# Kernel optimization log

Hardware: AMD Instinct MI355X
Metric: run time of the kernel (lower is better)

The kernel has to match this reference:

```python
import jax, jax.numpy as jnp
from jax import lax
import numpy as np

L, B, T, D, H = 4, 64, 256, 1024, 1024  # num_layers, batch, seq_len, input_dim, hidden_dim


def setup_inputs() -> dict:
    key = jax.random.key(0)
    ks = jax.random.split(key, 10)
    s = 0.05  # weight scale ~ xavier-ish for stability
    return {
        "x": jax.random.normal(ks[0], (B, T, D), jnp.float32),
        "hidden": jax.random.normal(ks[1], (L, B, H), jnp.float32),
        "cell": jax.random.normal(ks[2], (L, B, H), jnp.float32),
        # stacked per-layer LSTM params (layer0 input dim == H since D == H)
        "W_ih": jax.random.normal(ks[3], (L, 4 * H, H), jnp.float32) * s,
        "W_hh": jax.random.normal(ks[4], (L, 4 * H, H), jnp.float32) * s,
        "b": jax.random.normal(ks[5], (L, 4 * H), jnp.float32) * s,  # b_ih + b_hh combined
        "W_out": jax.random.normal(ks[6], (D, H), jnp.float32) * s,
        "b_out": jnp.zeros((D,), jnp.float32),
    }


def _lstm_layer(x_seq, h0, c0, Wih, Whh, b):
    """Run one LSTM layer over the full sequence.
    x_seq: [B,T,Din]; h0,c0: [B,H]. Returns hidden/cell sequences [B,T,H]."""
    # precompute input-side gate projections for all timesteps: [T,B,4H]
    gx = jnp.einsum('btd,gd->tbg', x_seq, Wih) + b

    def step(carry, gx_t):
        h, c = carry
        g = gx_t + h @ Whh.T  # [B,4H]
        i, f, gg, o = jnp.split(g, 4, axis=-1)  # torch gate order i,f,g,o
        c = jax.nn.sigmoid(f) * c + jax.nn.sigmoid(i) * jnp.tanh(gg)
        h = jax.nn.sigmoid(o) * jnp.tanh(c)
        return (h, c), (h, c)

    _, (hs, cs) = lax.scan(step, (h0, c0), gx)
    return jnp.swapaxes(hs, 0, 1), jnp.swapaxes(cs, 0, 1)  # [B,T,H]


def reference(x, hidden, cell, W_ih, W_hh, b, W_out, b_out):
    # dropout in eval mode (identity) for a deterministic reference
    out_h = x
    new_h, new_c = [], []
    for i in range(L):
        out_h, out_c = _lstm_layer(out_h, hidden[i], cell[i], W_ih[i], W_hh[i], b[i])
        new_h.append(out_h[:, -1])
        new_c.append(out_c[:, -1])
    logits = out_h @ W_out.T + b_out  # [B,T,D]
    return logits, (jnp.stack(new_h, axis=0), jnp.stack(new_c, axis=0))
```

## Files before the change

### kernel.cpp

```cpp
#include <hip/hip_runtime.h>
#include <cstdint>
#include <cstddef>


#define LL 4
#define BB 64
#define TT 256
#define DD 1024
#define HH 1024
#define FOURH 4096
#define APAD 1032
#define PPAD 68

typedef __bf16 bf16;
typedef __bf16 bf16x8 __attribute__((ext_vector_type(8)));
typedef __bf16 bf16x4 __attribute__((ext_vector_type(4)));
typedef __bf16 bf16x2 __attribute__((ext_vector_type(2)));
typedef float f32x4 __attribute__((ext_vector_type(4)));

__device__ __forceinline__ void async_load16(const void* g, void* l) {
    __builtin_amdgcn_global_load_lds(
        (const __attribute__((address_space(1))) unsigned int*)g,
        (__attribute__((address_space(3))) unsigned int*)l,
        16, 0, 0);
}

__device__ __forceinline__ f32x4 mfma_bf16(bf16x8 a, bf16x8 b, f32x4 c) {
    return __builtin_amdgcn_mfma_f32_16x16x32_bf16(a, b, c, 0, 0, 0);
}

__device__ __forceinline__ float fsig(float x) {
    return 1.f / (1.f + __expf(-x));
}
__device__ __forceinline__ float ftanh(float x) {
    x = fminf(10.f, fmaxf(-10.f, x));
    float e = __expf(2.f * x);
    return (e - 1.f) / (e + 1.f);
}

__device__ __forceinline__ int aload(const int* p) {
    return __hip_atomic_load(p, __ATOMIC_RELAXED, __HIP_MEMORY_SCOPE_AGENT);
}
__device__ __forceinline__ void astore(int* p, int v) {
    __hip_atomic_store(p, v, __ATOMIC_RELAXED, __HIP_MEMORY_SCOPE_AGENT);
}

__global__ void cvt_f32_bf16(const float* __restrict__ in, bf16* __restrict__ out, int n4) {
    int i = blockIdx.x * blockDim.x + threadIdx.x;
    if (i < n4) {
        float4 v = ((const float4*)in)[i];
        bf16x4 o = { (bf16)v.x, (bf16)v.y, (bf16)v.z, (bf16)v.w };
        ((bf16x4*)out)[i] = o;
    }
}

__global__ __launch_bounds__(256) void cvt_x_transpose(
    const float* __restrict__ x, bf16* __restrict__ out) {
    int bx = blockIdx.x;
    int b = bx >> 8, t = bx & 255;
    int tid = threadIdx.x;
    float4 v = ((const float4*)(x + (size_t)bx * DD))[tid];
    bf16x4 o = { (bf16)v.x, (bf16)v.y, (bf16)v.z, (bf16)v.w };
    ((bf16x4*)(out + ((size_t)(t * BB + b)) * DD))[tid] = o;
}

template <bool OUT_BF16, bool REMAP>
__global__ __launch_bounds__(256) void gemm_bt(
    const bf16* __restrict__ A, const bf16* __restrict__ W,
    const float* __restrict__ bias, void* __restrict__ Cout,
    int M, int N, int K)
{
    __shared__ bf16 As[128 * 32];
    __shared__ bf16 Bs[128 * 32];
    const int tid = threadIdx.x;
    const int wave = tid >> 6, lane = tid & 63;
    const int lmod = lane & 15, lhalf = lane >> 4;
    const int m0 = blockIdx.y * 128, n0 = blockIdx.x * 128;
    const int wr = (wave >> 1) * 64, wc = (wave & 1) * 64;

    f32x4 acc[4][4] = {};

    const int arow = tid >> 2;
    const int acol = (tid & 3) * 8;
    const bf16* Ab  = A + (size_t)(m0 + arow) * K + acol;
    const bf16* Ab2 = A + (size_t)(m0 + 64 + arow) * K + acol;
    const bf16* Wb  = W + (size_t)(n0 + arow) * K + acol;
    const bf16* Wb2 = W + (size_t)(n0 + 64 + arow) * K + acol;

    for (int kc = 0; kc < K; kc += 32) {
        async_load16(Ab + kc,  &As[tid * 8]);
        async_load16(Ab2 + kc, &As[2048 + tid * 8]);
        async_load16(Wb + kc,  &Bs[tid * 8]);
        async_load16(Wb2 + kc, &Bs[2048 + tid * 8]);
        __syncthreads();

        bf16x8 af[4], bfr[4];
#pragma unroll
        for (int mt = 0; mt < 4; mt++)
            af[mt] = *(const bf16x8*)&As[(wr + mt * 16 + lmod) * 32 + lhalf * 8];
#pragma unroll
        for (int nt = 0; nt < 4; nt++)
            bfr[nt] = *(const bf16x8*)&Bs[(wc + nt * 16 + lmod) * 32 + lhalf * 8];
#pragma unroll
        for (int mt = 0; mt < 4; mt++)
#pragma unroll
            for (int nt = 0; nt < 4; nt++)
                acc[mt][nt] = mfma_bf16(af[mt], bfr[nt], acc[mt][nt]);
        __syncthreads();
    }

#pragma unroll
    for (int mt = 0; mt < 4; mt++) {
#pragma unroll
        for (int nt = 0; nt < 4; nt++) {
            int n = n0 + wc + nt * 16 + lmod;
            float bv = bias[n];
#pragma unroll
            for (int r = 0; r < 4; r++) {
                int m = m0 + wr + mt * 16 + lhalf * 4 + r;
                int orow = REMAP ? ((m & 63) * TT + (m >> 6)) : m;
                float v = acc[mt][nt][r] + bv;
                if (OUT_BF16)
                    ((bf16*)Cout)[(size_t)orow * N + n] = (bf16)v;
                else
                    ((float*)Cout)[(size_t)orow * N + n] = v;
            }
        }
    }
}

__global__ __launch_bounds__(256, 1) void lstm_pipe(
    const bf16* __restrict__ x_bf,
    const bf16* __restrict__ h0_all,
    const float* __restrict__ c0_all,
    const bf16* __restrict__ wih,
    const bf16* __restrict__ whh,
    const float* __restrict__ bias,
    bf16* __restrict__ hseq_base,
    float* __restrict__ outH, float* __restrict__ outC,
    int* __restrict__ flags,
    int* __restrict__ mbox)
{
    __shared__ __align__(16) unsigned char smem_raw[64 * APAD * 2];
    bf16*  As = (bf16*)smem_raw;
    float* P  = (float*)smem_raw;

    const int tid = threadIdx.x;
    const int wave = tid >> 6, lane = tid & 63;
    const int lmod = lane & 15, lhalf = lane >> 4;
    const int bid = blockIdx.x;
    const int layer = bid >> 6;
    const int j0 = (bid & 63) * 16;
    const bool isAgg = ((bid & 63) == 0);

    const size_t SLAB = (size_t)TT * BB * HH;
    const bf16* inseq = (layer == 0) ? x_bf : (hseq_base + (size_t)(layer - 1) * SLAB);
    bf16* hseq = hseq_base + (size_t)layer * SLAB;
    const bf16* h0 = h0_all + (size_t)layer * BB * HH;
    const float* c0 = c0_all + (size_t)layer * BB * HH;
    float* oH = outH + (size_t)layer * BB * HH;
    float* oC = outC + (size_t)layer * BB * HH;

    bf16x8 wI[4][8], wH[4][8];
    {
        const size_t lbase = (size_t)layer * FOURH;
#pragma unroll
        for (int nt = 0; nt < 4; nt++) {
            const bf16* rI = wih + (lbase + nt * 1024 + j0 + lmod) * 1024
                                 + wave * 256 + lhalf * 8;
            const bf16* rH = whh + (lbase + nt * 1024 + j0 + lmod) * 1024
                                 + wave * 256 + lhalf * 8;
#pragma unroll
            for (int kc = 0; kc < 8; kc++) {
                wI[nt][kc] = *(const bf16x8*)(rI + kc * 32);
                wH[nt][kc] = *(const bf16x8*)(rH + kc * 32);
            }
        }
    }

    const int jj0 = (tid * 2) & 15;
    float bj[4][2];
#pragma unroll
    for (int g = 0; g < 4; g++) {
        bj[g][0] = bias[layer * FOURH + g * 1024 + j0 + jj0];
        bj[g][1] = bias[layer * FOURH + g * 1024 + j0 + jj0 + 1];
    }

    float2 creg[2];
#pragma unroll
    for (int q = 0; q < 2; q++) {
        int p = q * 512 + tid * 2;
        creg[q] = *(const float2*)&c0[(p >> 4) * 1024 + j0 + (p & 15)];
    }

    auto stage = [&](const bf16* src) {
#pragma unroll
        for (int i = 0; i < 32; i++) {
            int k = wave * 32 + i;
            int row = k >> 1, half = k & 1;
            async_load16(src + (size_t)row * 1024 + half * 512 + lane * 8,
                         &As[row * APAD + half * 512 + lane * 8]);
        }
    };

    for (int t = 0; t < TT; t++) {
        if (wave == 0) {
            if (isAgg && t > 0) {
                for (;;) {
                    int v = aload(&flags[layer * 64 + lane]);
                    if (__all(v >= t)) break;
                }
                astore(&mbox[(layer * 64 + lane) * 16 + 0], t);
                if (layer < 3)
                    astore(&mbox[((layer + 1) * 64 + lane) * 16 + 1], t);
            }
            if (layer > 0 && lane == 0) {
                while (aload(&mbox[bid * 16 + 1]) < t + 1) {}
            }
        }
        __syncthreads();

        stage(inseq + (size_t)t * (BB * HH));
        __syncthreads();

        f32x4 acc[4][4] = {};
#pragma unroll
        for (int kc = 0; kc < 8; kc++) {
            bf16x8 af[4];
#pragma unroll
            for (int mt = 0; mt < 4; mt++)
                af[mt] = *(const bf16x8*)&As[(mt * 16 + lmod) * APAD
                                             + wave * 256 + kc * 32 + lhalf * 8];
#pragma unroll
            for (int mt = 0; mt < 4; mt++)
#pragma unroll
                for (int nt = 0; nt < 4; nt++)
                    acc[mt][nt] = mfma_bf16(af[mt], wI[nt][kc], acc[mt][nt]);
        }

        if (wave == 0 && !isAgg && t > 0 && lane == 0) {
            while (aload(&mbox[bid * 16 + 0]) < t) {}
        }
        __syncthreads();

        stage((t == 0) ? h0 : (hseq + (size_t)(t - 1) * BB * HH));
        __syncthreads();

#pragma unroll
        for (int kc = 0; kc < 8; kc++) {
            bf16x8 af[4];
#pragma unroll
            for (int mt = 0; mt < 4; mt++)
                af[mt] = *(const bf16x8*)&As[(mt * 16 + lmod) * APAD
                                             + wave * 256 + kc * 32 + lhalf * 8];
#pragma unroll
            for (int mt = 0; mt < 4; mt++)
#pragma unroll
                for (int nt = 0; nt < 4; nt++)
                    acc[mt][nt] = mfma_bf16(af[mt], wH[nt][kc], acc[mt][nt]);
        }
        __syncthreads();

#pragma unroll
        for (int mt = 0; mt < 4; mt++)
#pragma unroll
            for (int nt = 0; nt < 4; nt++)
#pragma unroll
                for (int rr = 0; rr < 4; rr++) {
                    int m = mt * 16 + lhalf * 4 + rr;
                    P[(wave * 64 + m) * PPAD + nt * 16 + lmod] = acc[mt][nt][rr];
                }
        __syncthreads();

        const bool lastt = (t == TT - 1);
#pragma unroll
        for (int q = 0; q < 2; q++) {
            int p = q * 512 + tid * 2;
            int m = p >> 4, jj = p & 15;
            float gg4[4][2];
#pragma unroll
            for (int g = 0; g < 4; g++) {
                float s0 = bj[g][0], s1 = bj[g][1];
#pragma unroll
                for (int w = 0; w < 4; w++) {
                    float2 pv = *(const float2*)&P[(w * 64 + m) * PPAD + g * 16 + jj];
                    s0 += pv.x; s1 += pv.y;
                }
                gg4[g][0] = s0; gg4[g][1] = s1;
            }
            float cv[2], hv[2];
#pragma unroll
            for (int u = 0; u < 2; u++) {
                float gi = gg4[0][u], gf = gg4[1][u], gc = gg4[2][u], go = gg4[3][u];
                float cprev = u ? creg[q].y : creg[q].x;
                float c = fsig(gf) * cprev + fsig(gi) * ftanh(gc);
                float h = fsig(go) * ftanh(c);
                cv[u] = c; hv[u] = h;
            }
            creg[q].x = cv[0]; creg[q].y = cv[1];
            union { bf16x2 h2; unsigned int u32; } pk;
            pk.h2.x = (bf16)hv[0]; pk.h2.y = (bf16)hv[1];
            __hip_atomic_store(
                (unsigned int*)&hseq[((size_t)(t * BB + m)) * HH + j0 + jj],
                pk.u32, __ATOMIC_RELAXED, __HIP_MEMORY_SCOPE_AGENT);
            if (lastt) {
                *(float2*)&oH[m * 1024 + j0 + jj] = make_float2(hv[0], hv[1]);
                *(float2*)&oC[m * 1024 + j0 + jj] = make_float2(cv[0], cv[1]);
            }
        }

        __syncthreads();
        if (tid == 0) astore(&flags[bid], t + 1);
    }

    if (wave == 0 && isAgg && layer < 3) {
        for (;;) {
            int v = aload(&flags[layer * 64 + lane]);
            if (__all(v >= TT)) break;
        }
        astore(&mbox[((layer + 1) * 64 + lane) * 16 + 1], TT);
    }
}

extern "C" void kernel_launch(void* const* d_in, const int* in_sizes, int n_in,
                              void* d_out, int out_size, void* d_ws, size_t ws_size,
                              hipStream_t stream) {
    const float* x    = (const float*)d_in[0];
    const float* h0   = (const float*)d_in[1];
    const float* c0   = (const float*)d_in[2];
    const float* Wih  = (const float*)d_in[3];
    const float* Whh  = (const float*)d_in[4];
    const float* bias = (const float*)d_in[5];
    const float* Wout = (const float*)d_in[6];
    const float* bout = (const float*)d_in[7];

    char* p = (char*)d_ws;
    int*  ctrs    = (int*)p;  p += 1024;
    int*  mbox    = (int*)p;  p += 256 * 64;
    bf16* x_bf    = (bf16*)p; p += (size_t)BB * TT * DD * 2;
    bf16* hseq    = (bf16*)p; p += (size_t)LL * BB * TT * HH * 2;
    bf16* wih_bf  = (bf16*)p; p += (size_t)LL * FOURH * HH * 2;
    bf16* whh_bf  = (bf16*)p; p += (size_t)LL * FOURH * HH * 2;
    bf16* wout_bf = (bf16*)p; p += (size_t)DD * HH * 2;
    bf16* h0_bf   = (bf16*)p; p += (size_t)LL * BB * HH * 2;
    if ((size_t)(p - (char*)d_ws) > ws_size) return;

    hipMemsetAsync(ctrs, 0, 1024 + 256 * 64, stream);

    cvt_x_transpose<<<BB * TT, 256, 0, stream>>>(x, x_bf);
    {
        struct { const float* in; bf16* out; size_t n; } jobs[4] = {
            { Wih,  wih_bf,  (size_t)LL * FOURH * HH },
            { Whh,  whh_bf,  (size_t)LL * FOURH * HH },
            { Wout, wout_bf, (size_t)DD * HH },
            { h0,   h0_bf,   (size_t)LL * BB * HH },
        };
        for (int j = 0; j < 4; j++) {
            int n4 = (int)(jobs[j].n / 4);
            cvt_f32_bf16<<<(n4 + 255) / 256, 256, 0, stream>>>(jobs[j].in, jobs[j].out, n4);
        }
    }

    float* logits = (float*)d_out;
    float* outH = logits + (size_t)BB * TT * DD;
    float* outC = outH + (size_t)LL * BB * HH;

    lstm_pipe<<<LL * 64, 256, 0, stream>>>(
        x_bf, h0_bf, c0, wih_bf, whh_bf, bias,
        hseq, outH, outC, ctrs, mbox);

    dim3 g2(DD / 128, (BB * TT) / 128);
    gemm_bt<false, true><<<g2, 256, 0, stream>>>(
        hseq + (size_t)(LL - 1) * TT * BB * HH, wout_bf, bout, logits,
        BB * TT, DD, HH);
}
```

Before: 2.298 ms.

## Replace aggregator barrier with per-block flag broadcast and direct global A loads

```diff
diff --git a/kernel.cpp b/kernel.cpp
--- a/kernel.cpp
+++ b/kernel.cpp
@@ -9,7 +9,6 @@
 #define DD 1024
 #define HH 1024
 #define FOURH 4096
-#define APAD 1032
 #define PPAD 68
 
 typedef __bf16 bf16;
@@ -138,20 +137,18 @@
     const float* __restrict__ bias,
     bf16* __restrict__ hseq_base,
     float* __restrict__ outH, float* __restrict__ outC,
-    int* __restrict__ flags,
-    int* __restrict__ mbox)
+    int* __restrict__ sync)
 {
-    __shared__ __align__(16) unsigned char smem_raw[64 * APAD * 2];
-    bf16*  As = (bf16*)smem_raw;
-    float* P  = (float*)smem_raw;
+    __shared__ float P[5][64][PPAD];
+    float* Pf = &P[0][0][0];
 
     const int tid = threadIdx.x;
     const int wave = tid >> 6, lane = tid & 63;
     const int lmod = lane & 15, lhalf = lane >> 4;
     const int bid = blockIdx.x;
     const int layer = bid >> 6;
-    const int j0 = (bid & 63) * 16;
-    const bool isAgg = ((bid & 63) == 0);
+    const int blk = bid & 63;
+    const int j0 = blk * 16;
 
     const size_t SLAB = (size_t)TT * BB * HH;
     const bf16* inseq = (layer == 0) ? x_bf : (hseq_base + (size_t)(layer - 1) * SLAB);
@@ -161,6 +158,11 @@
     float* oH = outH + (size_t)layer * BB * HH;
     float* oC = outC + (size_t)layer * BB * HH;
 
+    int* myOwn = sync + bid * 128;
+    int* myIn  = sync + bid * 128 + 64;
+    int* peerOwnBase = sync + (size_t)(layer * 64) * 128 + blk;
+    int* nextInBase  = sync + (size_t)((layer + 1) * 64) * 128 + 64 + blk;
+
     bf16x8 wI[4][8], wH[4][8];
     {
         const size_t lbase = (size_t)layer * FOURH;
@@ -193,73 +195,64 @@
         creg[q] = *(const float2*)&c0[(p >> 4) * 1024 + j0 + (p & 15)];
     }
 
-    auto stage = [&](const bf16* src) {
-#pragma unroll
-        for (int i = 0; i < 32; i++) {
-            int k = wave * 32 + i;
-            int row = k >> 1, half = k & 1;
-            async_load16(src + (size_t)row * 1024 + half * 512 + lane * 8,
-                         &As[row * APAD + half * 512 + lane * 8]);
+    auto mmul = [&](const bf16* src, const bf16x8 (&W)[4][8], f32x4 (&acc)[4][4]) {
+        const bf16* b[4];
+#pragma unroll
+        for (int mt = 0; mt < 4; mt++)
+            b[mt] = src + (size_t)(mt * 16 + lmod) * 1024 + wave * 256 + lhalf * 8;
+        bf16x8 fA[2][4], fB[2][4];
+#pragma unroll
+        for (int h = 0; h < 2; h++)
+#pragma unroll
+            for (int mt = 0; mt < 4; mt++)
+                fA[h][mt] = *(const bf16x8*)(b[mt] + h * 32);
+#pragma unroll
+        for (int kp = 0; kp < 4; kp++) {
+            if (kp < 3) {
+#pragma unroll
+                for (int h = 0; h < 2; h++)
+#pragma unroll
+                    for (int mt = 0; mt < 4; mt++)
+                        fB[h][mt] = *(const bf16x8*)(b[mt] + ((kp + 1) * 2 + h) * 32);
+            }
+#pragma unroll
+            for (int h = 0; h < 2; h++)
+#pragma unroll
+                for (int mt = 0; mt < 4; mt++)
+#pragma unroll
+                    for (int nt = 0; nt < 4; nt++)
+                        acc[mt][nt] = mfma_bf16(fA[h][mt], W[nt][kp * 2 + h], acc[mt][nt]);
+#pragma unroll
+            for (int h = 0; h < 2; h++)
+#pragma unroll
+                for (int mt = 0; mt < 4; mt++)
+                    fA[h][mt] = fB[h][mt];
         }
     };
 
     for (int t = 0; t < TT; t++) {
-        if (wave == 0) {
-            if (isAgg && t > 0) {
-                for (;;) {
-                    int v = aload(&flags[layer * 64 + lane]);
-                    if (__all(v >= t)) break;
-                }
-                astore(&mbox[(layer * 64 + lane) * 16 + 0], t);
-                if (layer < 3)
-                    astore(&mbox[((layer + 1) * 64 + lane) * 16 + 1], t);
-            }
-            if (layer > 0 && lane == 0) {
-                while (aload(&mbox[bid * 16 + 1]) < t + 1) {}
-            }
-        }
-        __syncthreads();
-
-        stage(inseq + (size_t)t * (BB * HH));
-        __syncthreads();
+        if (layer > 0 && wave == 0) {
+            for (;;) {
+                int v = aload(&myIn[lane]);
+                if (__all(v >= t + 1)) break;
+            }
+        }
+        __syncthreads();
+        asm volatile("" ::: "memory");
 
         f32x4 acc[4][4] = {};
-#pragma unroll
-        for (int kc = 0; kc < 8; kc++) {
-            bf16x8 af[4];
-#pragma unroll
-            for (int mt = 0; mt < 4; mt++)
-                af[mt] = *(const bf16x8*)&As[(mt * 16 + lmod) * APAD
-                                             + wave * 256 + kc * 32 + lhalf * 8];
-#pragma unroll
-            for (int mt = 0; mt < 4; mt++)
-#pragma unroll
-                for (int nt = 0; nt < 4; nt++)
-                    acc[mt][nt] = mfma_bf16(af[mt], wI[nt][kc], acc[mt][nt]);
-        }
-
-        if (wave == 0 && !isAgg && t > 0 && lane == 0) {
-            while (aload(&mbox[bid * 16 + 0]) < t) {}
-        }
-        __syncthreads();
-
-        stage((t == 0) ? h0 : (hseq + (size_t)(t - 1) * BB * HH));
-        __syncthreads();
-
-#pragma unroll
-        for (int kc = 0; kc < 8; kc++) {
-            bf16x8 af[4];
-#pragma unroll
-            for (int mt = 0; mt < 4; mt++)
-                af[mt] = *(const bf16x8*)&As[(mt * 16 + lmod) * APAD
-                                             + wave * 256 + kc * 32 + lhalf * 8];
-#pragma unroll
-            for (int mt = 0; mt < 4; mt++)
-#pragma unroll
-                for (int nt = 0; nt < 4; nt++)
-                    acc[mt][nt] = mfma_bf16(af[mt], wH[nt][kc], acc[mt][nt]);
-        }
-        __syncthreads();
+        mmul(inseq + (size_t)t * (BB * HH), wI, acc);
+
+        if (t > 0 && wave == 0) {
+            for (;;) {
+                int v = aload(&myOwn[lane]);
+                if (__all(v >= t)) break;
+            }
+        }
+        __syncthreads();
+        asm volatile("" ::: "memory");
+
+        mmul((t == 0) ? h0 : (hseq + (size_t)(t - 1) * BB * HH), wH, acc);
 
 #pragma unroll
         for (int mt = 0; mt < 4; mt++)
@@ -268,7 +261,7 @@
 #pragma unroll
                 for (int rr = 0; rr < 4; rr++) {
                     int m = mt * 16 + lhalf * 4 + rr;
-                    P[(wave * 64 + m) * PPAD + nt * 16 + lmod] = acc[mt][nt][rr];
+                    Pf[(wave * 64 + m) * PPAD + nt * 16 + lmod] = acc[mt][nt][rr];
                 }
         __syncthreads();
 
@@ -283,7 +276,7 @@
                 float s0 = bj[g][0], s1 = bj[g][1];
 #pragma unroll
                 for (int w = 0; w < 4; w++) {
-                    float2 pv = *(const float2*)&P[(w * 64 + m) * PPAD + g * 16 + jj];
+                    float2 pv = *(const float2*)&Pf[(w * 64 + m) * PPAD + g * 16 + jj];
                     s0 += pv.x; s1 += pv.y;
                 }
                 gg4[g][0] = s0; gg4[g][1] = s1;
@@ -310,15 +303,11 @@
         }
 
         __syncthreads();
-        if (tid == 0) astore(&flags[bid], t + 1);
-    }
-
-    if (wave == 0 && isAgg && layer < 3) {
-        for (;;) {
-            int v = aload(&flags[layer * 64 + lane]);
-            if (__all(v >= TT)) break;
-        }
-        astore(&mbox[((layer + 1) * 64 + lane) * 16 + 1], TT);
+        if (wave == 0) {
+            astore(peerOwnBase + (size_t)lane * 128, t + 1);
+            if (layer < 3)
+                astore(nextInBase + (size_t)lane * 128, t + 1);
+        }
     }
 }
 
@@ -335,8 +324,7 @@
     const float* bout = (const float*)d_in[7];
 
     char* p = (char*)d_ws;
-    int*  ctrs    = (int*)p;  p += 1024;
-    int*  mbox    = (int*)p;  p += 256 * 64;
+    int*  sync    = (int*)p;  p += 256 * 128 * 4;
     bf16* x_bf    = (bf16*)p; p += (size_t)BB * TT * DD * 2;
     bf16* hseq    = (bf16*)p; p += (size_t)LL * BB * TT * HH * 2;
     bf16* wih_bf  = (bf16*)p; p += (size_t)LL * FOURH * HH * 2;
@@ -345,7 +333,7 @@
     bf16* h0_bf   = (bf16*)p; p += (size_t)LL * BB * HH * 2;
     if ((size_t)(p - (char*)d_ws) > ws_size) return;
 
-    hipMemsetAsync(ctrs, 0, 1024 + 256 * 64, stream);
+    hipMemsetAsync(sync, 0, 256 * 128 * 4, stream);
 
     cvt_x_transpose<<<BB * TT, 256, 0, stream>>>(x, x_bf);
     {
@@ -367,7 +355,7 @@
 
     lstm_pipe<<<LL * 64, 256, 0, stream>>>(
         x_bf, h0_bf, c0, wih_bf, whh_bf, bias,
-        hseq, outH, outC, ctrs, mbox);
+        hseq, outH, outC, sync);
 
     dim3 g2(DD / 128, (BB * TT) / 128);
     gemm_bt<false, true><<<g2, 256, 0, stream>>>(
```

Result: slower. 4.416 ms (+92.2%).
